# Optimization experiments

Measured on AMD Instinct MI355X. Metric: run time of the kernel, lower is better.

The kernel has to match this reference:

```python
import jax, jax.numpy as jnp
import numpy as np

BIG_GAMMA = 1e10  # sentinel distance for the last sample, as in the torch code
EPS = 1e-10


def _exclusive_cumprod(x):
    # cumprod shifted right by one with a leading 1 along the last axis
    cp = jnp.cumprod(x, axis=-1)
    return jnp.concatenate([jnp.ones_like(cp[..., :1]), cp[..., :-1]], axis=-1)


def setup_inputs() -> dict:
    key = jax.random.key(0)
    k1, k2, k3 = jax.random.split(key, 3)
    B, R, S = 1, 65536, 128
    radiance_field = jax.random.normal(k1, (B, R, S, 4), dtype=jnp.float32)
    ray_directions = jax.random.normal(k2, (B, R, 3), dtype=jnp.float32)
    ray_depth_samples = jax.random.uniform(k3, (B, R, S), dtype=jnp.float32)
    return {
        "radiance_field": radiance_field,
        "ray_directions": ray_directions,
        "ray_depth_samples": ray_depth_samples,
        "include_weights": 1,
    }


def reference(radiance_field, ray_directions, ray_depth_samples, include_weights):
    # gammas: distance between adjacent depth samples, huge value for the last one
    gammas = jnp.concatenate(
        [ray_depth_samples[..., 1:] - ray_depth_samples[..., :-1],
         jnp.full_like(ray_depth_samples[..., :1], BIG_GAMMA)],
        axis=-1,
    )  # (B, R, S)
    # scale by ray direction norm (one direction per ray, broadcast over samples)
    dir_norm = jnp.linalg.norm(ray_directions, axis=-1, keepdims=True)  # (B, R, 1)
    gammas = gammas * dir_norm

    rgb = radiance_field[..., :3]          # (B, R, S, 3)
    sigmas = radiance_field[..., 3]        # (B, R, S)

    alpha = 1.0 - jnp.exp(-sigmas * gammas)            # (B, R, S)
    T = _exclusive_cumprod(1.0 - alpha + EPS)          # (B, R, S)
    weights = T * alpha                                # (B, R, S)
    out_rgb = jnp.sum(weights[..., None] * rgb, axis=-2)  # (B, R, 3)

    if include_weights:
        return (out_rgb, weights)
    return out_rgb
```

## Files before the change

### kernel.cpp

```cpp
#include <hip/hip_runtime.h>
#include <math.h>


#define BIG_GAMMA_F 1e10f
#define EPS_W 1e-10f

constexpr int S = 128;

__global__ __launch_bounds__(256) void volrender_kernel(
    const float* __restrict__ rf,
    const float* __restrict__ dirs,
    const float* __restrict__ depth,
    float* __restrict__ out_rgb,
    float* __restrict__ out_w,
    int R)
{
    const int lane = threadIdx.x & 63;
    const int ray  = (blockIdx.x * blockDim.x + threadIdx.x) >> 6;
    if (ray >= R) return;

    const float dx = dirs[ray * 3 + 0];
    const float dy = dirs[ray * 3 + 1];
    const float dz = dirs[ray * 3 + 2];
    const float dn = sqrtf(dx * dx + dy * dy + dz * dz);

    const float4* __restrict__ rfp = (const float4*)rf + (size_t)ray * S;
    const float*  __restrict__ dpp = depth + (size_t)ray * S;

    const float4 rA = rfp[lane];
    const float4 rB = rfp[lane + 64];
    const float  dA = dpp[lane];
    const float  dB = dpp[lane + 64];

    const float dA_next = __shfl_down(dA, 1, 64);
    const float dB_next = __shfl_down(dB, 1, 64);
    const float d64     = __shfl(dB, 0, 64);

    float grawA = (lane < 63) ? (dA_next - dA) : (d64 - dA);
    float grawB = (lane < 63) ? (dB_next - dB) : BIG_GAMMA_F;

    const float gA = grawA * dn;
    const float gB = grawB * dn;

    const float alphaA = 1.0f - expf(-rA.w * gA);
    const float alphaB = 1.0f - expf(-rB.w * gB);
    const float uA = (1.0f - alphaA) + EPS_W;
    const float uB = (1.0f - alphaB) + EPS_W;

    float SA = uA;
    #pragma unroll
    for (int d = 1; d < 64; d <<= 1) {
        const float t = __shfl_up(SA, d, 64);
        if (lane >= d) SA *= t;
    }
    float SB = uB;
    #pragma unroll
    for (int d = 1; d < 64; d <<= 1) {
        const float t = __shfl_up(SB, d, 64);
        if (lane >= d) SB *= t;
    }

    const float exA = __shfl_up(SA, 1, 64);
    const float TA  = (lane == 0) ? 1.0f : exA;
    const float P1  = __shfl(SA, 63, 64);
    const float exB = __shfl_up(SB, 1, 64);
    const float TB  = P1 * ((lane == 0) ? 1.0f : exB);

    float wA = TA * alphaA;
    float wB = TB * alphaB;
    if (!isfinite(wA)) wA = 0.0f;
    if (!isfinite(wB)) wB = 0.0f;

    float* __restrict__ owp = out_w + (size_t)ray * S;
    owp[lane]      = wA;
    owp[lane + 64] = wB;

    float Sr = wA * rA.x + wB * rB.x;
    float Sg = wA * rA.y + wB * rB.y;
    float Sb = wA * rA.z + wB * rB.z;
    #pragma unroll
    for (int d = 1; d < 64; d <<= 1) {
        Sr += __shfl_xor(Sr, d, 64);
        Sg += __shfl_xor(Sg, d, 64);
        Sb += __shfl_xor(Sb, d, 64);
    }
    if (lane < 3) {
        float v = (lane == 0) ? Sr : (lane == 1) ? Sg : Sb;
        if (!isfinite(v)) v = 0.0f;
        out_rgb[ray * 3 + lane] = v;
    }
}

extern "C" void kernel_launch(void* const* d_in, const int* in_sizes, int n_in,
                              void* d_out, int out_size, void* d_ws, size_t ws_size,
                              hipStream_t stream) {
    const float* rf    = (const float*)d_in[0];
    const float* dirs  = (const float*)d_in[1];
    const float* depth = (const float*)d_in[2];

    int R = in_sizes[1] / 3;
    float* out_rgb = (float*)d_out;
    float* out_w   = (float*)d_out + (size_t)R * 3;

    const int block = 256;
    const long long threads_total = (long long)R * 64;
    const int grid = (int)((threads_total + block - 1) / block);
    volrender_kernel<<<grid, block, 0, stream>>>(rf, dirs, depth, out_rgb, out_w, R);
}
```

Measured before the change: 223.0 us.

## Process four rays per wave with double-buffered prefetch and nontemporal weight stores

Each wavefront now handles several rays in a grid-stride pattern and issues the loads for the next ray before computing the current one. This software pipelining is meant to hide global-memory latency. The two prefix-product scans are interleaved to expose more instruction-level parallelism, and the weight stores use nontemporal hints. The cost is higher register pressure and a quarter as many waves in flight, which may reduce the latency hiding that occupancy provided before.

Result: slower. 227.7 us (+2.1%).

```diff
diff --git a/kernel.cpp b/kernel.cpp
--- a/kernel.cpp
+++ b/kernel.cpp
@@ -6,6 +6,7 @@
 #define EPS_W 1e-10f
 
 constexpr int S = 128;
+constexpr int RPW = 4;
 
 __global__ __launch_bounds__(256) void volrender_kernel(
     const float* __restrict__ rf,
@@ -15,80 +16,99 @@
     float* __restrict__ out_w,
     int R)
 {
-    const int lane = threadIdx.x & 63;
-    const int ray  = (blockIdx.x * blockDim.x + threadIdx.x) >> 6;
-    if (ray >= R) return;
+    const int lane   = threadIdx.x & 63;
+    const int wave   = (blockIdx.x * blockDim.x + threadIdx.x) >> 6;
+    const int nwaves = (gridDim.x * blockDim.x) >> 6;
 
-    const float dx = dirs[ray * 3 + 0];
-    const float dy = dirs[ray * 3 + 1];
-    const float dz = dirs[ray * 3 + 2];
-    const float dn = sqrtf(dx * dx + dy * dy + dz * dz);
+    float4 rA[2], rB[2];
+    float  dA[2], dB[2];
+    float  dvx[2], dvy[2], dvz[2];
 
-    const float4* __restrict__ rfp = (const float4*)rf + (size_t)ray * S;
-    const float*  __restrict__ dpp = depth + (size_t)ray * S;
+    #define ISSUE_LOADS(ray, b)                                           \
+        do {                                                              \
+            const float4* __restrict__ rfp =                              \
+                (const float4*)rf + (size_t)(ray) * S;                    \
+            const float* __restrict__ dpp = depth + (size_t)(ray) * S;    \
+            rA[b] = rfp[lane];                                            \
+            rB[b] = rfp[lane + 64];                                       \
+            dA[b] = dpp[lane];                                            \
+            dB[b] = dpp[lane + 64];                                       \
+            dvx[b] = dirs[(ray) * 3 + 0];                                 \
+            dvy[b] = dirs[(ray) * 3 + 1];                                 \
+            dvz[b] = dirs[(ray) * 3 + 2];                                 \
+        } while (0)
 
-    const float4 rA = rfp[lane];
-    const float4 rB = rfp[lane + 64];
-    const float  dA = dpp[lane];
-    const float  dB = dpp[lane + 64];
+    const int ray0 = wave;
+    if (ray0 < R) ISSUE_LOADS(ray0, 0);
 
-    const float dA_next = __shfl_down(dA, 1, 64);
-    const float dB_next = __shfl_down(dB, 1, 64);
-    const float d64     = __shfl(dB, 0, 64);
+    #pragma unroll
+    for (int k = 0; k < RPW; ++k) {
+        const int cur = k & 1;
+        const int ray = wave + k * nwaves;
+        if (ray >= R) break;
 
-    float grawA = (lane < 63) ? (dA_next - dA) : (d64 - dA);
-    float grawB = (lane < 63) ? (dB_next - dB) : BIG_GAMMA_F;
+        const int nray = wave + (k + 1) * nwaves;
+        if (k + 1 < RPW && nray < R) ISSUE_LOADS(nray, cur ^ 1);
 
-    const float gA = grawA * dn;
-    const float gB = grawB * dn;
+        const float dn = sqrtf(dvx[cur] * dvx[cur] + dvy[cur] * dvy[cur] +
+                               dvz[cur] * dvz[cur]);
 
-    const float alphaA = 1.0f - expf(-rA.w * gA);
-    const float alphaB = 1.0f - expf(-rB.w * gB);
-    const float uA = (1.0f - alphaA) + EPS_W;
-    const float uB = (1.0f - alphaB) + EPS_W;
+        const float4 ra = rA[cur];
+        const float4 rb = rB[cur];
+        const float  da = dA[cur];
+        const float  db = dB[cur];
 
-    float SA = uA;
-    #pragma unroll
-    for (int d = 1; d < 64; d <<= 1) {
-        const float t = __shfl_up(SA, d, 64);
-        if (lane >= d) SA *= t;
+        const float da_next = __shfl_down(da, 1, 64);
+        const float db_next = __shfl_down(db, 1, 64);
+        const float d64     = __shfl(db, 0, 64);
+
+        const float grawA = (lane < 63) ? (da_next - da) : (d64 - da);
+        const float grawB = (lane < 63) ? (db_next - db) : BIG_GAMMA_F;
+
+        const float alphaA = 1.0f - expf(-ra.w * (grawA * dn));
+        const float alphaB = 1.0f - expf(-rb.w * (grawB * dn));
+        const float uA = (1.0f - alphaA) + EPS_W;
+        const float uB = (1.0f - alphaB) + EPS_W;
+
+        float SA = uA, SB = uB;
+        #pragma unroll
+        for (int d = 1; d < 64; d <<= 1) {
+            const float tA = __shfl_up(SA, d, 64);
+            const float tB = __shfl_up(SB, d, 64);
+            if (lane >= d) { SA *= tA; SB *= tB; }
+        }
+
+        const float exA = __shfl_up(SA, 1, 64);
+        const float TA  = (lane == 0) ? 1.0f : exA;
+        const float P1  = __shfl(SA, 63, 64);
+        const float exB = __shfl_up(SB, 1, 64);
+        const float TB  = P1 * ((lane == 0) ? 1.0f : exB);
+
+        float wAv = TA * alphaA;
+        float wBv = TB * alphaB;
+        if (!isfinite(wAv)) wAv = 0.0f;
+        if (!isfinite(wBv)) wBv = 0.0f;
+
+        float* __restrict__ owp = out_w + (size_t)ray * S;
+        __builtin_nontemporal_store(wAv, &owp[lane]);
+        __builtin_nontemporal_store(wBv, &owp[lane + 64]);
+
+        float Sr = wAv * ra.x + wBv * rb.x;
+        float Sg = wAv * ra.y + wBv * rb.y;
+        float Sb = wAv * ra.z + wBv * rb.z;
+        #pragma unroll
+        for (int d = 1; d < 64; d <<= 1) {
+            Sr += __shfl_xor(Sr, d, 64);
+            Sg += __shfl_xor(Sg, d, 64);
+            Sb += __shfl_xor(Sb, d, 64);
+        }
+        if (lane < 3) {
+            float v = (lane == 0) ? Sr : (lane == 1) ? Sg : Sb;
+            if (!isfinite(v)) v = 0.0f;
+            out_rgb[ray * 3 + lane] = v;
+        }
     }
-    float SB = uB;
-    #pragma unroll
-    for (int d = 1; d < 64; d <<= 1) {
-        const float t = __shfl_up(SB, d, 64);
-        if (lane >= d) SB *= t;
-    }
-
-    const float exA = __shfl_up(SA, 1, 64);
-    const float TA  = (lane == 0) ? 1.0f : exA;
-    const float P1  = __shfl(SA, 63, 64);
-    const float exB = __shfl_up(SB, 1, 64);
-    const float TB  = P1 * ((lane == 0) ? 1.0f : exB);
-
-    float wA = TA * alphaA;
-    float wB = TB * alphaB;
-    if (!isfinite(wA)) wA = 0.0f;
-    if (!isfinite(wB)) wB = 0.0f;
-
-    float* __restrict__ owp = out_w + (size_t)ray * S;
-    owp[lane]      = wA;
-    owp[lane + 64] = wB;
-
-    float Sr = wA * rA.x + wB * rB.x;
-    float Sg = wA * rA.y + wB * rB.y;
-    float Sb = wA * rA.z + wB * rB.z;
-    #pragma unroll
-    for (int d = 1; d < 64; d <<= 1) {
-        Sr += __shfl_xor(Sr, d, 64);
-        Sg += __shfl_xor(Sg, d, 64);
-        Sb += __shfl_xor(Sb, d, 64);
-    }
-    if (lane < 3) {
-        float v = (lane == 0) ? Sr : (lane == 1) ? Sg : Sb;
-        if (!isfinite(v)) v = 0.0f;
-        out_rgb[ray * 3 + lane] = v;
-    }
+    #undef ISSUE_LOADS
 }
 
 extern "C" void kernel_launch(void* const* d_in, const int* in_sizes, int n_in,
@@ -103,7 +123,8 @@
     float* out_w   = (float*)d_out + (size_t)R * 3;
 
     const int block = 256;
-    const long long threads_total = (long long)R * 64;
+    const int waves = (R + RPW - 1) / RPW;
+    const long long threads_total = (long long)waves * 64;
     const int grid = (int)((threads_total + block - 1) / block);
     volrender_kernel<<<grid, block, 0, stream>>>(rf, dirs, depth, out_rgb, out_w, R);
 }
```

## Switch to one ray per thread with chunked LDS staging and serial transmittance

Applied to the files above, without the earlier changes.

The kernel now assigns one ray per thread in 64-thread blocks. It stages 8-sample chunks of radiance and depth gaps through swizzled shared memory, prefetching the next chunk into registers while the current chunk is computed. Transmittance becomes a sequential running product per thread, which removes the cross-lane shuffle scans and reductions. Weights are written back as 16-byte nontemporal stores. The trade-off is a small block size with two barriers per chunk and heavy register use (staging buffers plus 32 weight registers), which may reduce occupancy.

Result: slower. 261.4 us (+17.3%).

```diff
diff --git a/kernel.cpp b/kernel.cpp
--- a/kernel.cpp
+++ b/kernel.cpp
@@ -5,9 +5,15 @@
 #define BIG_GAMMA_F 1e10f
 #define EPS_W 1e-10f
 
-constexpr int S = 128;
+typedef float floatx4 __attribute__((ext_vector_type(4)));
 
-__global__ __launch_bounds__(256) void volrender_kernel(
+constexpr int S   = 128;
+constexpr int RPB = 64;
+constexpr int CH  = 8;
+constexpr int NCH = S / CH;
+constexpr int GST = 9;
+
+__global__ __launch_bounds__(64) void volrender_kernel(
     const float* __restrict__ rf,
     const float* __restrict__ dirs,
     const float* __restrict__ depth,
@@ -15,80 +21,94 @@
     float* __restrict__ out_w,
     int R)
 {
-    const int lane = threadIdx.x & 63;
-    const int ray  = (blockIdx.x * blockDim.x + threadIdx.x) >> 6;
-    if (ray >= R) return;
+    const int t    = threadIdx.x;
+    const int rayb = blockIdx.x * RPB;
+    const int ray  = rayb + t;
+    if (rayb >= R) return;
+
+    __shared__ floatx4 s_rf[RPB * CH];
+    __shared__ float   s_g [RPB * GST];
 
     const float dx = dirs[ray * 3 + 0];
     const float dy = dirs[ray * 3 + 1];
     const float dz = dirs[ray * 3 + 2];
     const float dn = sqrtf(dx * dx + dy * dy + dz * dz);
 
-    const float4* __restrict__ rfp = (const float4*)rf + (size_t)ray * S;
-    const float*  __restrict__ dpp = depth + (size_t)ray * S;
+    const int sub = t & 7;
+    const int rg  = t >> 3;
 
-    const float4 rA = rfp[lane];
-    const float4 rB = rfp[lane + 64];
-    const float  dA = dpp[lane];
-    const float  dB = dpp[lane + 64];
+    floatx4 st_rf[CH];
+    float   st_g [CH];
 
-    const float dA_next = __shfl_down(dA, 1, 64);
-    const float dB_next = __shfl_down(dB, 1, 64);
-    const float d64     = __shfl(dB, 0, 64);
+    auto issue = [&](int c) {
+        #pragma unroll
+        for (int i = 0; i < CH; ++i) {
+            const int    r    = i * 8 + rg;
+            const size_t base = (size_t)(rayb + r) * S;
+            const int    gs   = c * CH + sub;
+            st_rf[i] = ((const floatx4*)rf)[base + gs];
+            const float d0 = depth[base + gs];
+            st_g[i] = (gs < S - 1) ? (depth[base + gs + 1] - d0)
+                                   : BIG_GAMMA_F;
+        }
+    };
+    auto commit = [&]() {
+        #pragma unroll
+        for (int i = 0; i < CH; ++i) {
+            const int r = i * 8 + rg;
+            s_rf[r * CH + (sub ^ (r & 7))] = st_rf[i];
+            s_g [r * GST + sub]            = st_g[i];
+        }
+    };
 
-    float grawA = (lane < 63) ? (dA_next - dA) : (d64 - dA);
-    float grawB = (lane < 63) ? (dB_next - dB) : BIG_GAMMA_F;
+    issue(0);
+    commit();
+    __syncthreads();
 
-    const float gA = grawA * dn;
-    const float gB = grawB * dn;
+    float T  = 1.0f;
+    float Sr = 0.0f, Sg = 0.0f, Sb = 0.0f;
 
-    const float alphaA = 1.0f - expf(-rA.w * gA);
-    const float alphaB = 1.0f - expf(-rB.w * gB);
-    const float uA = (1.0f - alphaA) + EPS_W;
-    const float uB = (1.0f - alphaB) + EPS_W;
+    for (int cg = 0; cg < NCH / 4; ++cg) {
+        float wreg[32];
+        #pragma unroll
+        for (int cc = 0; cc < 4; ++cc) {
+            const int  c       = cg * 4 + cc;
+            const bool notlast = (c < NCH - 1);
+            if (notlast) issue(c + 1);
 
-    float SA = uA;
-    #pragma unroll
-    for (int d = 1; d < 64; d <<= 1) {
-        const float t = __shfl_up(SA, d, 64);
-        if (lane >= d) SA *= t;
-    }
-    float SB = uB;
-    #pragma unroll
-    for (int d = 1; d < 64; d <<= 1) {
-        const float t = __shfl_up(SB, d, 64);
-        if (lane >= d) SB *= t;
+            #pragma unroll
+            for (int s = 0; s < CH; ++s) {
+                const floatx4 f4   = s_rf[t * CH + (s ^ (t & 7))];
+                const float   graw = s_g [t * GST + s];
+                const float   gamma = graw * dn;
+                const float   alpha = 1.0f - expf(-f4.w * gamma);
+                float w = T * alpha;
+                if (!isfinite(w)) w = 0.0f;
+                wreg[cc * CH + s] = w;
+                Sr += w * f4.x;
+                Sg += w * f4.y;
+                Sb += w * f4.z;
+                T *= (1.0f - alpha) + EPS_W;
+            }
+            __syncthreads();
+            if (notlast) commit();
+            __syncthreads();
+        }
+        floatx4* owp = (floatx4*)(out_w + (size_t)ray * S) + cg * 8;
+        #pragma unroll
+        for (int q = 0; q < 8; ++q) {
+            floatx4 v = { wreg[q * 4 + 0], wreg[q * 4 + 1],
+                          wreg[q * 4 + 2], wreg[q * 4 + 3] };
+            __builtin_nontemporal_store(v, &owp[q]);
+        }
     }
 
-    const float exA = __shfl_up(SA, 1, 64);
-    const float TA  = (lane == 0) ? 1.0f : exA;
-    const float P1  = __shfl(SA, 63, 64);
-    const float exB = __shfl_up(SB, 1, 64);
-    const float TB  = P1 * ((lane == 0) ? 1.0f : exB);
-
-    float wA = TA * alphaA;
-    float wB = TB * alphaB;
-    if (!isfinite(wA)) wA = 0.0f;
-    if (!isfinite(wB)) wB = 0.0f;
-
-    float* __restrict__ owp = out_w + (size_t)ray * S;
-    owp[lane]      = wA;
-    owp[lane + 64] = wB;
-
-    float Sr = wA * rA.x + wB * rB.x;
-    float Sg = wA * rA.y + wB * rB.y;
-    float Sb = wA * rA.z + wB * rB.z;
-    #pragma unroll
-    for (int d = 1; d < 64; d <<= 1) {
-        Sr += __shfl_xor(Sr, d, 64);
-        Sg += __shfl_xor(Sg, d, 64);
-        Sb += __shfl_xor(Sb, d, 64);
-    }
-    if (lane < 3) {
-        float v = (lane == 0) ? Sr : (lane == 1) ? Sg : Sb;
-        if (!isfinite(v)) v = 0.0f;
-        out_rgb[ray * 3 + lane] = v;
-    }
+    if (!isfinite(Sr)) Sr = 0.0f;
+    if (!isfinite(Sg)) Sg = 0.0f;
+    if (!isfinite(Sb)) Sb = 0.0f;
+    out_rgb[ray * 3 + 0] = Sr;
+    out_rgb[ray * 3 + 1] = Sg;
+    out_rgb[ray * 3 + 2] = Sb;
 }
 
 extern "C" void kernel_launch(void* const* d_in, const int* in_sizes, int n_in,
@@ -102,8 +122,6 @@
     float* out_rgb = (float*)d_out;
     float* out_w   = (float*)d_out + (size_t)R * 3;
 
-    const int block = 256;
-    const long long threads_total = (long long)R * 64;
-    const int grid = (int)((threads_total + block - 1) / block);
-    volrender_kernel<<<grid, block, 0, stream>>>(rf, dirs, depth, out_rgb, out_w, R);
+    const int grid = (R + RPB - 1) / RPB;
+    volrender_kernel<<<grid, RPB, 0, stream>>>(rf, dirs, depth, out_rgb, out_w, R);
 }
```

## Process multiple rays per wave with prefetching and contiguous sample pairs

Applied to the files above, without the earlier changes.

Each wavefront now handles 8 rays in sequence and double-buffers the loads for the next ray while computing the current one, so memory latency overlaps compute. Each lane now owns two adjacent samples instead of samples lane and lane+64. That allows vectorized float2 depth loads and weight stores, and cuts the product scan to a single 64-lane pass per ray. It also switches to the fast __expf. The trade-offs are more registers per thread, fewer waves in flight, and slightly lower exp precision.

New measurement: 232.5 us. +4.3%, slower.

```diff
diff --git a/kernel.cpp b/kernel.cpp
--- a/kernel.cpp
+++ b/kernel.cpp
@@ -5,7 +5,10 @@
 #define BIG_GAMMA_F 1e10f
 #define EPS_W 1e-10f
 
-constexpr int S = 128;
+typedef float floatx2 __attribute__((ext_vector_type(2)));
+
+constexpr int S   = 128;
+constexpr int RPW = 8;
 
 __global__ __launch_bounds__(256) void volrender_kernel(
     const float* __restrict__ rf,
@@ -16,79 +19,87 @@
     int R)
 {
     const int lane = threadIdx.x & 63;
-    const int ray  = (blockIdx.x * blockDim.x + threadIdx.x) >> 6;
-    if (ray >= R) return;
+    const int wave = (blockIdx.x * blockDim.x + threadIdx.x) >> 6;
 
-    const float dx = dirs[ray * 3 + 0];
-    const float dy = dirs[ray * 3 + 1];
-    const float dz = dirs[ray * 3 + 2];
-    const float dn = sqrtf(dx * dx + dy * dy + dz * dz);
+    const int ray0 = wave * RPW;
+    if (ray0 >= R) return;
 
-    const float4* __restrict__ rfp = (const float4*)rf + (size_t)ray * S;
-    const float*  __restrict__ dpp = depth + (size_t)ray * S;
+    float4  rE[2], rO[2];
+    floatx2 dp[2];
+    float   dvx[2], dvy[2], dvz[2];
 
-    const float4 rA = rfp[lane];
-    const float4 rB = rfp[lane + 64];
-    const float  dA = dpp[lane];
-    const float  dB = dpp[lane + 64];
+    #define ISSUE(ray, b)                                                  \
+        do {                                                               \
+            const float4* __restrict__ rfp =                               \
+                (const float4*)rf + (size_t)(ray) * S + 2 * lane;          \
+            rE[b] = rfp[0];                                                \
+            rO[b] = rfp[1];                                                \
+            dp[b] = *((const floatx2*)(depth + (size_t)(ray) * S) + lane); \
+            dvx[b] = dirs[(ray) * 3 + 0];                                  \
+            dvy[b] = dirs[(ray) * 3 + 1];                                  \
+            dvz[b] = dirs[(ray) * 3 + 2];                                  \
+        } while (0)
 
-    const float dA_next = __shfl_down(dA, 1, 64);
-    const float dB_next = __shfl_down(dB, 1, 64);
-    const float d64     = __shfl(dB, 0, 64);
+    ISSUE(ray0, 0);
 
-    float grawA = (lane < 63) ? (dA_next - dA) : (d64 - dA);
-    float grawB = (lane < 63) ? (dB_next - dB) : BIG_GAMMA_F;
+    #pragma unroll
+    for (int k = 0; k < RPW; ++k) {
+        const int cur = k & 1;
+        const int ray = ray0 + k;
+        if (ray >= R) break;
 
-    const float gA = grawA * dn;
-    const float gB = grawB * dn;
+        if (k + 1 < RPW && ray + 1 < R) ISSUE(ray + 1, cur ^ 1);
 
-    const float alphaA = 1.0f - expf(-rA.w * gA);
-    const float alphaB = 1.0f - expf(-rB.w * gB);
-    const float uA = (1.0f - alphaA) + EPS_W;
-    const float uB = (1.0f - alphaB) + EPS_W;
+        const float dn = sqrtf(dvx[cur] * dvx[cur] + dvy[cur] * dvy[cur] +
+                               dvz[cur] * dvz[cur]);
 
-    float SA = uA;
-    #pragma unroll
-    for (int d = 1; d < 64; d <<= 1) {
-        const float t = __shfl_up(SA, d, 64);
-        if (lane >= d) SA *= t;
+        const float4 re = rE[cur];
+        const float4 ro = rO[cur];
+        const float  dE = dp[cur].x;
+        const float  dO = dp[cur].y;
+
+        const float dNext = __shfl_down(dE, 1, 64);
+        const float gE = (dO - dE) * dn;
+        const float gO = ((lane < 63) ? (dNext - dO) : BIG_GAMMA_F) * dn;
+
+        const float aE = 1.0f - __expf(-re.w * gE);
+        const float aO = 1.0f - __expf(-ro.w * gO);
+        const float uE = (1.0f - aE) + EPS_W;
+        const float uO = (1.0f - aO) + EPS_W;
+
+        float Sv = uE * uO;
+        #pragma unroll
+        for (int d = 1; d < 64; d <<= 1) {
+            const float t = __shfl_up(Sv, d, 64);
+            if (lane >= d) Sv *= t;
+        }
+        const float ex = __shfl_up(Sv, 1, 64);
+        const float Tb = (lane == 0) ? 1.0f : ex;
+
+        float wE = Tb * aE;
+        float wO = (Tb * uE) * aO;
+        if (!isfinite(wE)) wE = 0.0f;
+        if (!isfinite(wO)) wO = 0.0f;
+
+        floatx2 wst = { wE, wO };
+        *((floatx2*)(out_w + (size_t)ray * S) + lane) = wst;
+
+        float Sr = wE * re.x + wO * ro.x;
+        float Sg = wE * re.y + wO * ro.y;
+        float Sb = wE * re.z + wO * ro.z;
+        #pragma unroll
+        for (int d = 1; d < 64; d <<= 1) {
+            Sr += __shfl_xor(Sr, d, 64);
+            Sg += __shfl_xor(Sg, d, 64);
+            Sb += __shfl_xor(Sb, d, 64);
+        }
+        if (lane < 3) {
+            float v = (lane == 0) ? Sr : (lane == 1) ? Sg : Sb;
+            if (!isfinite(v)) v = 0.0f;
+            out_rgb[ray * 3 + lane] = v;
+        }
     }
-    float SB = uB;
-    #pragma unroll
-    for (int d = 1; d < 64; d <<= 1) {
-        const float t = __shfl_up(SB, d, 64);
-        if (lane >= d) SB *= t;
-    }
-
-    const float exA = __shfl_up(SA, 1, 64);
-    const float TA  = (lane == 0) ? 1.0f : exA;
-    const float P1  = __shfl(SA, 63, 64);
-    const float exB = __shfl_up(SB, 1, 64);
-    const float TB  = P1 * ((lane == 0) ? 1.0f : exB);
-
-    float wA = TA * alphaA;
-    float wB = TB * alphaB;
-    if (!isfinite(wA)) wA = 0.0f;
-    if (!isfinite(wB)) wB = 0.0f;
-
-    float* __restrict__ owp = out_w + (size_t)ray * S;
-    owp[lane]      = wA;
-    owp[lane + 64] = wB;
-
-    float Sr = wA * rA.x + wB * rB.x;
-    float Sg = wA * rA.y + wB * rB.y;
-    float Sb = wA * rA.z + wB * rB.z;
-    #pragma unroll
-    for (int d = 1; d < 64; d <<= 1) {
-        Sr += __shfl_xor(Sr, d, 64);
-        Sg += __shfl_xor(Sg, d, 64);
-        Sb += __shfl_xor(Sb, d, 64);
-    }
-    if (lane < 3) {
-        float v = (lane == 0) ? Sr : (lane == 1) ? Sg : Sb;
-        if (!isfinite(v)) v = 0.0f;
-        out_rgb[ray * 3 + lane] = v;
-    }
+    #undef ISSUE
 }
 
 extern "C" void kernel_launch(void* const* d_in, const int* in_sizes, int n_in,
@@ -103,7 +114,8 @@
     float* out_w   = (float*)d_out + (size_t)R * 3;
 
     const int block = 256;
-    const long long threads_total = (long long)R * 64;
+    const int waves = (R + RPW - 1) / RPW;
+    const long long threads_total = (long long)waves * 64;
     const int grid = (int)((threads_total + block - 1) / block);
     volrender_kernel<<<grid, block, 0, stream>>>(rf, dirs, depth, out_rgb, out_w, R);
 }
```
